# Optimization experiments

Measured on AMD Instinct MI355X. Metric: run time of the kernel, lower is better.

The kernel has to match this reference:

```python
import jax, jax.numpy as jnp
import numpy as np
from jax import lax

sg = lax.stop_gradient

# (kernel, stride, pad, pool_k, pool_s) for the 7 conv blocks
CFG = [(16, 2, 7, 8, 4), (12, 2, 5, 4, 2), (9, 1, 4, 5, 2), (7, 1, 3, 4, 2),
       (5, 1, 2, 2, 2), (3, 1, 1, 2, 2), (3, 1, 1, 2, 2)]
W_SHAPES = [(8, 1, 16), (12, 8, 12), (32, 12, 9), (64, 32, 7),
            (64, 64, 5), (64, 64, 3), (72, 64, 3)]
CH = [8, 12, 32, 64, 64, 64, 72]


def bin_act(x):
    # forward: sign(x); backward: clipped-quadratic surrogate (STE)
    s = jnp.sign(x)
    le = (x < -1.0).astype(x.dtype)
    ri = (x >= 1.0).astype(x.dtype)
    cl = ((x >= -1.0) & (x < 0.0)).astype(x.dtype)
    cr = ((x >= 0.0) & (x < 1.0)).astype(x.dtype)
    out = cl * (2.0 + x) * x + cr * (2.0 - x) * x + ri - le
    return sg(s) + out - sg(out)


def bin_wei(w, axes):
    # forward: scale * sign(w) with scale = mean|w| (detached); backward through tanh (STE)
    scale = sg(jnp.mean(jnp.abs(w), axis=axes, keepdims=True))
    t = jnp.tanh(w)
    return sg(scale * jnp.sign(w)) + t - sg(t)


def conv1d(x, w, stride, pad):
    return lax.conv_general_dilated(x, w, (stride,), [(pad, pad)],
                                    dimension_numbers=('NCH', 'OIH', 'NCH'))


def maxpool1d(x, k, s):
    return lax.reduce_window(x, -jnp.inf, lax.max, (1, 1, k), (1, 1, s), 'VALID')


def batchnorm1d(x, gamma, beta, eps=1e-5):
    # training-mode BN: batch statistics over (N, L), biased variance
    m = jnp.mean(x, axis=(0, 2), keepdims=True)
    v = jnp.mean((x - m) ** 2, axis=(0, 2), keepdims=True)
    return gamma[None, :, None] * (x - m) / jnp.sqrt(v + eps) + beta[None, :, None]


def _forward(x, ws, gs, bs, wfc):
    for w, g, b, (k, s, p, pk, ps) in zip(ws, gs, bs, CFG):
        x = conv1d(x, bin_wei(w, (1, 2)), s, p)
        x = maxpool1d(x, pk, ps)
        x = batchnorm1d(x, g, b)
        x = bin_act(x)
    x = x.reshape(x.shape[0], -1)                 # [B, 72*3]
    return x @ bin_wei(wfc, (1,)).T               # [B, classCount]


def setup_inputs() -> dict:
    key = jax.random.key(0)
    ks = jax.random.split(key, 9)
    inp = {'x': jax.random.normal(ks[0], (2048, 1, 3600), dtype=jnp.float32)}
    for i, shp in enumerate(W_SHAPES):
        inp[f'w{i+1}'] = jax.random.uniform(ks[i + 1], shp, dtype=jnp.float32) * 0.32
        inp[f'g{i+1}'] = jnp.ones((CH[i],), jnp.float32)
        inp[f'b{i+1}'] = jnp.zeros((CH[i],), jnp.float32)
    inp['wfc'] = jax.random.uniform(ks[8], (5, 216), dtype=jnp.float32) * 0.32
    return inp


def reference(x, w1, w2, w3, w4, w5, w6, w7,
              g1, g2, g3, g4, g5, g6, g7,
              b1, b2, b3, b4, b5, b6, b7, wfc):
    ws = [w1, w2, w3, w4, w5, w6, w7]
    gs = [g1, g2, g3, g4, g5, g6, g7]
    bs = [b1, b2, b3, b4, b5, b6, b7]
    return _forward(x, ws, gs, bs, wfc)
```

## Files before the change

### kernel.cpp

```cpp
#include <hip/hip_runtime.h>
#include <math.h>
#include <stdint.h>

#define NBATCH 2048
#define NSLOT 32

struct Args {
    const float* x;
    const float* W[7];
    const float* G[7];
    const float* Bt[7];
    const float* WFC;
    float* out;
    float* bufA;
    float* bufB;
    double* stats;
    float* wsc;
    uint32_t* wmb;
};

__device__ __forceinline__ float signf(float v) {
    return (v > 0.f) ? 1.f : ((v < 0.f) ? -1.f : 0.f);
}

__global__ __launch_bounds__(256) void k_setup(Args a) {
    const int blk = blockIdx.x, tid = threadIdx.x;
    for (int i = blk * 256 + tid; i < NSLOT * 632; i += 391 * 256) a.stats[i] = 0.0;

    if (blk < 321 && tid < 64) {
        const int cum[9] = {0,8,20,52,116,180,244,316,321};
        const int per[8] = {16,96,108,224,320,192,192,216};
        const float* wsrc[8] = {a.W[0],a.W[1],a.W[2],a.W[3],a.W[4],a.W[5],a.W[6],a.WFC};
        int o = blk, L = 0;
        while (L < 7 && o >= cum[L + 1]) ++L;
        const int oo = o - cum[L], p = per[L];
        const float* wo = wsrc[L] + (size_t)oo * p;
        float s = 0.f;
        for (int i = tid; i < p; i += 64) s += fabsf(wo[i]);
        #pragma unroll
        for (int off = 32; off; off >>= 1) s += __shfl_down(s, off);
        if (tid == 0) a.wsc[o] = s / (float)p;
    }

    const int gid = (blk - 384) * 256 + tid;
    if (blk >= 384 && blk <= 388 && gid >= 0 && gid < 1176) {
        const int cum[5]  = {0,448,768,960,1176};
        const int cin[4]  = {32,64,64,64};
        const int kk[4]   = {7,5,3,3};
        const int wpp[4]  = {1,2,2,2};
        const int woff[4] = {356,804,1444,1828};
        const float* wsrc[4] = {a.W[3],a.W[4],a.W[5],a.W[6]};
        int L = 0;
        while (L < 3 && gid >= cum[L + 1]) ++L;
        const int idx = gid - cum[L];
        const int K = kk[L], CIN = cin[L], WPP = wpp[L];
        const int o = idx / K, k = idx - o * K;
        const float* w = wsrc[L];
        uint32_t m0 = 0, m1 = 0;
        for (int c = 0; c < CIN; ++c) {
            const float v = w[((size_t)o * CIN + c) * K + k];
            const uint32_t bit = (v < 0.f) ? 1u : 0u;
            int bp = c;
            if (CIN == 64) bp = 16 * (c & 3) + (c >> 2);
            else if (CIN == 32) bp = 8 * (c & 3) + (c >> 2);
            if (bp < 32) m0 |= bit << bp; else m1 |= bit << (bp - 32);
        }
        uint32_t* dst = a.wmb + woff[L] + (size_t)idx * WPP;
        dst[0] = m0;
        if (WPP == 2) dst[1] = m1;
    }

    if (blk == 389 && tid < 12) {
        const float* w = a.W[1];
        const int o = tid;
        #pragma unroll
        for (int g = 0; g < 3; ++g) {
            uint32_t word = 0;
            #pragma unroll
            for (int j = 0; j < 4; ++j) {
                const int k = 4 * g + j;
                uint32_t by = 0;
                #pragma unroll
                for (int c = 0; c < 8; ++c)
                    by |= (w[((size_t)o * 8 + c) * 12 + k] < 0.f ? 1u : 0u) << c;
                word |= by << (8 * j);
            }
            a.wmb[o * 3 + g] = word;
        }
    }
    if (blk == 390 && tid < 64) {
        const float* w = a.W[2];
        const int o = tid >> 1, ph = tid & 1;
        uint32_t mk[9];
        #pragma unroll
        for (int k = 0; k < 9; ++k) {
            uint32_t m = 0;
            #pragma unroll
            for (int c = 0; c < 12; ++c)
                m |= (w[((size_t)o * 12 + c) * 9 + k] < 0.f ? 1u : 0u) << c;
            mk[k] = m;
        }
        uint32_t wd[5];
        if (ph == 0) { wd[0]=mk[0]|(mk[1]<<16); wd[1]=mk[2]|(mk[3]<<16);
                       wd[2]=mk[4]|(mk[5]<<16); wd[3]=mk[6]|(mk[7]<<16); wd[4]=mk[8]; }
        else         { wd[0]=mk[0]<<16; wd[1]=mk[1]|(mk[2]<<16);
                       wd[2]=mk[3]|(mk[4]<<16); wd[3]=mk[5]|(mk[6]<<16); wd[4]=mk[7]|(mk[8]<<16); }
        #pragma unroll
        for (int g = 0; g < 5; ++g) a.wmb[36 + o * 10 + ph * 5 + g] = wd[g];
    }
}

__global__ __launch_bounds__(256) void k_conv1(Args a) {
    __shared__ float wgs[128];
    __shared__ double sred[16];
    const int n = blockIdx.x, tid = threadIdx.x, l = tid & 63;
    if (tid < 128) wgs[tid] = signf(a.W[0][tid]);
    if (tid < 16)  sred[tid] = 0.0;
    __syncthreads();
    const int r = tid;
    const float* xn = a.x + (size_t)n * 3600;
    float m0[8], m1[8];
    #pragma unroll
    for (int ch = 0; ch < 8; ++ch) { m0[ch] = 0.f; m1[ch] = 0.f; }
    if (r < 225) {
        float f[40];
        const int g0 = 16 * r - 8;
        #pragma unroll
        for (int b = 0; b < 10; ++b) {
            const int gg = g0 + 4 * b;
            if (gg >= 0 && gg <= 3596) {
                const float4 v = *(const float4*)(xn + gg);
                f[4*b] = v.x; f[4*b+1] = v.y; f[4*b+2] = v.z; f[4*b+3] = v.w;
            } else {
                f[4*b] = 0.f; f[4*b+1] = 0.f; f[4*b+2] = 0.f; f[4*b+3] = 0.f;
            }
        }
        #pragma unroll
        for (int ch = 0; ch < 8; ++ch) {
            float acc[12];
            #pragma unroll
            for (int j = 0; j < 12; ++j) acc[j] = 0.f;
            #pragma unroll
            for (int k = 0; k < 16; ++k) {
                const float wk = wgs[ch * 16 + k];
                #pragma unroll
                for (int j = 0; j < 12; ++j)
                    acc[j] = fmaf(f[2*j + 1 + k], wk, acc[j]);
            }
            const float lo  = fmaxf(fmaxf(acc[0], acc[1]), fmaxf(acc[2], acc[3]));
            const float mid = fmaxf(fmaxf(acc[4], acc[5]), fmaxf(acc[6], acc[7]));
            const float hi  = fmaxf(fmaxf(acc[8], acc[9]), fmaxf(acc[10], acc[11]));
            const float sc = a.wsc[ch];
            m0[ch] = fmaxf(lo, mid) * sc;
            m1[ch] = (r < 224) ? fmaxf(mid, hi) * sc : 0.f;
        }
        float* on = a.bufA + ((size_t)n * 449 + 2 * r) * 8;
        *(float4*)(on + 0) = make_float4(m0[0], m0[1], m0[2], m0[3]);
        *(float4*)(on + 4) = make_float4(m0[4], m0[5], m0[6], m0[7]);
        if (r < 224) {
            *(float4*)(on + 8)  = make_float4(m1[0], m1[1], m1[2], m1[3]);
            *(float4*)(on + 12) = make_float4(m1[4], m1[5], m1[6], m1[7]);
        }
    }
    #pragma unroll
    for (int ch = 0; ch < 8; ++ch) {
        double sS = (double)m0[ch] + (double)m1[ch];
        double s2 = (double)m0[ch] * m0[ch] + (double)m1[ch] * m1[ch];
        #pragma unroll
        for (int off = 32; off; off >>= 1) {
            sS += __shfl_down(sS, off);
            s2 += __shfl_down(s2, off);
        }
        if (l == 0) {
            atomicAdd(&sred[ch], sS);
            atomicAdd(&sred[8 + ch], s2);
        }
    }
    __syncthreads();
    if (tid < 16) {
        double* so = a.stats + (size_t)(n & (NSLOT - 1)) * 16;
        atomicAdd(&so[tid], sred[tid]);
    }
}

template <int CIN, int LIN, int O, int K, int STRIDE, int PAD,
          int PK, int PS, int LP, int WPP, int LPB, bool SF64>
__device__ __forceinline__ void bin_body(
    const float* __restrict__ xprev, const uint32_t* __restrict__ wm,
    const float* __restrict__ wsc, const float* __restrict__ wsc_prev,
    const double* __restrict__ stats_in,
    const float* __restrict__ gamma, const float* __restrict__ beta,
    const double cntInv, float* __restrict__ out, double* __restrict__ stats_out)
{
    constexpr int OL    = (O < 64) ? O : 64;
    constexpr int PO    = 64 / OL;
    constexpr int SPAN  = (PK - 1) * STRIDE + K;
    constexpr int QLEN  = 4 * LPB * PS * STRIDE + SPAN;
    constexpr int XM64A =
        (WPP == 2)   ? (QLEN + 2)
      : (CIN == 8)   ? ((QLEN + 48) + 7) / 8
      : (CIN == 12)  ? ((2 * (QLEN + 10)) + 7) / 8
      : ((QLEN + 2 + 3) / 2 + 1);
    constexpr int F     = 2 * CIN;
    constexpr int FW    = (F > 64) ? 128 : 64;

    __shared__ uint64_t xmbuf[XM64A];
    __shared__ long long foldU[4][FW];
    __shared__ int sS[4][O], sS2[4][O];

    const int tid = threadIdx.x;
    const int wv  = tid >> 6;
    const int l   = tid & 63;
    uint32_t* xm32 = (uint32_t*)xmbuf;
    uint64_t* xm64 = xmbuf;
    uint16_t* xm16 = (uint16_t*)xmbuf;
    uint8_t*  xm8  = (uint8_t*)xmbuf;

    const int n    = blockIdx.x;
    const int lp0b = blockIdx.y * (4 * LPB);
    const int lp1b = (lp0b + 4 * LPB < LP) ? lp0b + 4 * LPB : LP;
    const int q0raw = lp0b * PS * STRIDE - PAD;
    const int q0 = (q0raw > 0) ? q0raw : 0;
    const int q1raw = (lp1b - 1) * PS * STRIDE - PAD + SPAN;
    const int q1 = (q1raw < LIN) ? q1raw : LIN;
    int xbase;
    if constexpr (CIN == 8)       xbase = q0 & ~3;
    else if constexpr (CIN == 12) xbase = q0 - (q0 & 1);
    else if constexpr (WPP == 1)  xbase = q0 - ((q0 + (PAD & 1)) & 1);
    else                          xbase = q0;

    const int lp0 = lp0b + wv * LPB;
    const int lp1 = (lp0 + LPB < lp1b) ? lp0 + LPB : lp1b;

    const float* xn = xprev + (size_t)n * LIN * CIN;

    {
        const long long* stI = (const long long*)stats_in;
        long long pa = 0, pb_ = 0;
        double da = 0.0;
        #pragma unroll
        for (int s8 = 0; s8 < 8; ++s8) {
            const int s = (wv << 3) + s8;
            if constexpr (SF64) {
                if (l < F) da += stats_in[s * F + l];
            } else {
                if (l < ((F < 64) ? F : 64)) pa += stI[s * F + l];
                if constexpr (F > 64) { if (l < F - 64) pb_ += stI[s * F + 64 + l]; }
            }
        }
        if constexpr (SF64) foldU[wv][l] = __double_as_longlong(da);
        else {
            foldU[wv][l] = pa;
            if constexpr (F > 64) foldU[wv][64 + l] = pb_;
        }
    }
    __syncthreads();
    float aA = 0.f, aB = 0.f;
    {
        double t0 = 0.0, t1 = 0.0;
        if constexpr (SF64) {
            double tot = 0.0;
            #pragma unroll
            for (int w = 0; w < 4; ++w) tot += __longlong_as_double(foldU[w][l]);
            t0 = tot;
            t1 = __shfl(tot, CIN + l);
        } else if constexpr (F > 64) {
            long long a0 = 0, a1 = 0;
            #pragma unroll
            for (int w = 0; w < 4; ++w) { a0 += foldU[w][l]; a1 += foldU[w][64 + l]; }
            t0 = (double)a0; t1 = (double)a1;
        } else {
            long long a0 = 0;
            #pragma unroll
            for (int w = 0; w < 4; ++w) a0 += foldU[w][l];
            const double tot = (double)a0;
            t0 = tot;
            t1 = __shfl(tot, CIN + l);
        }
        if (l < CIN) {
            double mean, E2;
            if constexpr (SF64) { mean = t0 * cntInv; E2 = t1 * cntInv; }
            else {
                const double w = (double)wsc_prev[l];
                mean = w * t0 * cntInv; E2 = w * w * t1 * cntInv;
            }
            const double var = E2 - mean * mean;
            const double inv = 1.0 / sqrt(var + 1e-5);
            const double av  = (double)gamma[l] * inv;
            aA = (float)av;
            aB = (float)((double)beta[l] - mean * av);
        }
    }

    if constexpr (CIN == 64) {
        const int sub = l & 15, grp = l >> 4;
        const float a0 = __shfl(aA, 4*sub),     b0 = __shfl(aB, 4*sub);
        const float a1 = __shfl(aA, 4*sub + 1), b1 = __shfl(aB, 4*sub + 1);
        const float a2 = __shfl(aA, 4*sub + 2), b2 = __shfl(aB, 4*sub + 2);
        const float a3 = __shfl(aA, 4*sub + 3), b3 = __shfl(aB, 4*sub + 3);
        for (int pb = q0 + wv * 4; pb < q1; pb += 16) {
            const int pos = pb + grp;
            const bool valid = pos < q1;
            const float4 v = *(const float4*)(xn + (size_t)(valid ? pos : q0) * 64 + 4*sub);
            const unsigned long long bal0 = __ballot(valid && (fmaf(a0, v.x, b0) < 0.f));
            const unsigned long long bal1 = __ballot(valid && (fmaf(a1, v.y, b1) < 0.f));
            const unsigned long long bal2 = __ballot(valid && (fmaf(a2, v.z, b2) < 0.f));
            const unsigned long long bal3 = __ballot(valid && (fmaf(a3, v.w, b3) < 0.f));
            if (l < 4 && pb + l < q1) {
                const uint64_t m = ((bal0 >> (16*l)) & 0xFFFFull)
                                 | (((bal1 >> (16*l)) & 0xFFFFull) << 16)
                                 | (((bal2 >> (16*l)) & 0xFFFFull) << 32)
                                 | (((bal3 >> (16*l)) & 0xFFFFull) << 48);
                xm64[pb + l - xbase] = m;
            }
        }
    } else if constexpr (CIN == 32) {
        const int sub = l & 7, grp = l >> 3;
        const float a0 = __shfl(aA, 4*sub),     b0 = __shfl(aB, 4*sub);
        const float a1 = __shfl(aA, 4*sub + 1), b1 = __shfl(aB, 4*sub + 1);
        const float a2 = __shfl(aA, 4*sub + 2), b2 = __shfl(aB, 4*sub + 2);
        const float a3 = __shfl(aA, 4*sub + 3), b3 = __shfl(aB, 4*sub + 3);
        for (int pb = q0 + wv * 8; pb < q1; pb += 32) {
            const int pos = pb + grp;
            const bool valid = pos < q1;
            const float4 v = *(const float4*)(xn + (size_t)(valid ? pos : q0) * 32 + 4*sub);
            const unsigned long long bal0 = __ballot(valid && (fmaf(a0, v.x, b0) < 0.f));
            const unsigned long long bal1 = __ballot(valid && (fmaf(a1, v.y, b1) < 0.f));
            const unsigned long long bal2 = __ballot(valid && (fmaf(a2, v.z, b2) < 0.f));
            const unsigned long long bal3 = __ballot(valid && (fmaf(a3, v.w, b3) < 0.f));
            if (l < 8 && pb + l < q1) {
                const uint32_t m = (uint32_t)((bal0 >> (8*l)) & 0xFFull)
                                 | ((uint32_t)((bal1 >> (8*l)) & 0xFFull) << 8)
                                 | ((uint32_t)((bal2 >> (8*l)) & 0xFFull) << 16)
                                 | ((uint32_t)((bal3 >> (8*l)) & 0xFFull) << 24);
                xm32[pb + l - xbase] = m;
            }
        }
    } else if constexpr (CIN == 8) {
        const int sub = l & 1, grp = l >> 1;
        const float a0 = __shfl(aA, 4*sub),     b0 = __shfl(aB, 4*sub);
        const float a1 = __shfl(aA, 4*sub + 1), b1 = __shfl(aB, 4*sub + 1);
        const float a2 = __shfl(aA, 4*sub + 2), b2 = __shfl(aB, 4*sub + 2);
        const float a3 = __shfl(aA, 4*sub + 3), b3 = __shfl(aB, 4*sub + 3);
        for (int pb = q0 + wv * 32; pb < q1; pb += 128) {
            const int pos = pb + grp;
            const bool valid = pos < q1;
            const float4 v = *(const float4*)(xn + (size_t)(valid ? pos : q0) * 8 + 4*sub);
            const unsigned long long bal0 = __ballot(valid && (fmaf(a0, v.x, b0) < 0.f));
            const unsigned long long bal1 = __ballot(valid && (fmaf(a1, v.y, b1) < 0.f));
            const unsigned long long bal2 = __ballot(valid && (fmaf(a2, v.z, b2) < 0.f));
            const unsigned long long bal3 = __ballot(valid && (fmaf(a3, v.w, b3) < 0.f));
            if (l < 32 && pb + l < q1) {
                const uint32_t t0 = (uint32_t)((bal0 >> (2*l)) & 3ull);
                const uint32_t t1 = (uint32_t)((bal1 >> (2*l)) & 3ull);
                const uint32_t t2 = (uint32_t)((bal2 >> (2*l)) & 3ull);
                const uint32_t t3 = (uint32_t)((bal3 >> (2*l)) & 3ull);
                const uint32_t m = (t0 & 1) | ((t1 & 1) << 1) | ((t2 & 1) << 2) | ((t3 & 1) << 3)
                                 | ((t0 >> 1) << 4) | ((t1 >> 1) << 5) | ((t2 >> 1) << 6) | ((t3 >> 1) << 7);
                xm8[pb + l - xbase] = (uint8_t)m;
            }
        }
    } else {
        constexpr int PPW = 64 / CIN;
        const int pw = l / CIN, c = l - pw * CIN;
        const float myA = __shfl(aA, c), myB = __shfl(aB, c);
        const bool lact = (pw < PPW);
        for (int pb = q0 + wv * PPW; pb < q1; pb += 4 * PPW) {
            const int pos = pb + pw;
            const bool act = lact && (pos < q1);
            float v = 0.f;
            if (act) v = fmaf(myA, xn[(size_t)pb * CIN + l], myB);
            const unsigned long long bal = __ballot(act && (v < 0.f));
            if (act && c == 0) {
                const uint32_t mk = (uint32_t)((bal >> (pw * CIN)) & ((1u << CIN) - 1));
                xm16[pos - xbase] = (uint16_t)mk;
            }
        }
    }
    __syncthreads();

    float* on = out + (size_t)n * LP * O;

    if constexpr (WPP == 2) {
        const uint64_t* wmp = (const uint64_t*)wm;
        uint64_t wr[K];
        #pragma unroll
        for (int k = 0; k < K; ++k) wr[k] = wmp[l * K + k];
        uint64_t wr2[K];
        const int oo2 = 64 + ((O > 64 && l < O - 64) ? l : 0);
        if constexpr (O > 64) {
            #pragma unroll
            for (int k = 0; k < K; ++k) wr2[k] = wmp[oo2 * K + k];
        }
        const float myws  = wsc[l];
        const float myws2 = (O > 64 && l < O - 64) ? wsc[64 + l] : 0.f;
        int accS = 0, accS2 = 0, accSb = 0, accS2b = 0;

        for (int lp = lp0; lp < lp1; ++lp) {
            const int lo = lp * PS * STRIDE - PAD;
            int m = -1000000, m2 = -1000000;
            if (lo >= 0 && lo + SPAN <= LIN) {
                uint64_t tw[SPAN];
                #pragma unroll
                for (int t = 0; t < SPAN; ++t) tw[t] = xm64[lo - xbase + t];
                #pragma unroll
                for (int j = 0; j < PK; ++j) {
                    int p = 0;
                    #pragma unroll
                    for (int k = 0; k < K; ++k)
                        p += __popcll(tw[j * STRIDE + k] ^ wr[k]);
                    m = max(m, CIN * K - 2 * p);
                    if constexpr (O > 64) {
                        int p2 = 0;
                        #pragma unroll
                        for (int k = 0; k < K; ++k)
                            p2 += __popcll(tw[j * STRIDE + k] ^ wr2[k]);
                        m2 = max(m2, CIN * K - 2 * p2);
                    }
                }
            } else {
                #pragma unroll
                for (int j = 0; j < PK; ++j) {
                    const int base = lo + j * STRIDE;
                    int p = 0, nv = 0, p2 = 0;
                    #pragma unroll
                    for (int k = 0; k < K; ++k) {
                        const int q = base + k;
                        if (q >= 0 && q < LIN) {
                            ++nv;
                            const uint64_t xv = xm64[q - xbase];
                            p += __popcll(xv ^ wr[k]);
                            if constexpr (O > 64) p2 += __popcll(xv ^ wr2[k]);
                        }
                    }
                    m = max(m, CIN * nv - 2 * p);
                    if constexpr (O > 64) m2 = max(m2, CIN * nv - 2 * p2);
                }
            }
            on[lp * O + l] = (float)m * myws;
            accS += m; accS2 += m * m;
            if constexpr (O > 64) {
                if (l < O - 64) {
                    on[lp * O + 64 + l] = (float)m2 * myws2;
                    accSb += m2; accS2b += m2 * m2;
                }
            }
        }
        sS[wv][l] = accS; sS2[wv][l] = accS2;
        if constexpr (O > 64) {
            if (l < O - 64) { sS[wv][64 + l] = accSb; sS2[wv][64 + l] = accS2b; }
        }
    } else if constexpr (CIN == 8) {
        const int po = l / OL, oo = l - po * OL;
        const bool cact = (po < PO);
        const float myws = cact ? wsc[oo] : 0.f;
        const int osel = cact ? oo : 0;
        const uint32_t wr0 = wm[osel*3], wr1 = wm[osel*3+1], wr2 = wm[osel*3+2];
        uint32_t wb[12];
        #pragma unroll
        for (int k = 0; k < 12; ++k)
            wb[k] = ((k < 4 ? wr0 : (k < 8 ? wr1 : wr2)) >> (8 * (k & 3))) & 255u;
        const uint32_t* xw = (const uint32_t*)xmbuf;
        int accS = 0, accS2 = 0;

        for (int lp = lp0 + po; lp < lp1; lp += PO) {
            const int lo = lp * PS * STRIDE - PAD;
            int m = -1000000;
            if (lo >= 0 && lo + SPAN <= LIN) {
                const int bb = lo - xbase;
                const int w0 = bb >> 2;
                uint32_t tw[6];
                #pragma unroll
                for (int i = 0; i < 6; ++i) tw[i] = xw[w0 + i];
                #pragma unroll
                for (int j = 0; j < PK; ++j) {
                    const int wo = (j + 1) >> 1;
                    uint32_t e0, e1, e2;
                    if (j & 1) {
                        e0 = (tw[wo]   >> 8) | (tw[wo+1] << 24);
                        e1 = (tw[wo+1] >> 8) | (tw[wo+2] << 24);
                        e2 = (tw[wo+2] >> 8) | (tw[wo+3] << 24);
                    } else {
                        e0 = (tw[wo]   >> 24) | (tw[wo+1] << 8);
                        e1 = (tw[wo+1] >> 24) | (tw[wo+2] << 8);
                        e2 = (tw[wo+2] >> 24) | (tw[wo+3] << 8);
                    }
                    const int p = __popc(e0 ^ wr0) + __popc(e1 ^ wr1) + __popc(e2 ^ wr2);
                    m = max(m, 96 - 2 * p);
                }
            } else {
                #pragma unroll
                for (int j = 0; j < PK; ++j) {
                    const int base = lo + j * STRIDE;
                    int p = 0, nv = 0;
                    #pragma unroll
                    for (int k = 0; k < 12; ++k) {
                        const int q = base + k;
                        if (q >= 0 && q < LIN) { ++nv; p += __popc((uint32_t)xm8[q - xbase] ^ wb[k]); }
                    }
                    m = max(m, 8 * nv - 2 * p);
                }
            }
            if (cact) {
                on[lp * O + oo] = (float)m * myws;
                accS += m; accS2 += m * m;
            }
        }
        int t = accS, t2 = accS2;
        #pragma unroll
        for (int g = 1; g < PO; ++g) {
            t  += __shfl(accS,  l + g * OL);
            t2 += __shfl(accS2, l + g * OL);
        }
        if (l < OL) { sS[wv][l] = t; sS2[wv][l] = t2; }
    } else if constexpr (CIN == 12) {
        const int po = l / OL, oo = l - po * OL;
        const bool cact = (po < PO);
        const float myws = cact ? wsc[oo] : 0.f;
        const int osel = cact ? oo : 0;
        uint32_t wE[5], wO[5];
        #pragma unroll
        for (int g = 0; g < 5; ++g) { wE[g] = wm[osel*10 + g]; wO[g] = wm[osel*10 + 5 + g]; }
        uint32_t we16[9];
        we16[0]=wE[0]&0xFFFFu; we16[1]=wE[0]>>16; we16[2]=wE[1]&0xFFFFu; we16[3]=wE[1]>>16;
        we16[4]=wE[2]&0xFFFFu; we16[5]=wE[2]>>16; we16[6]=wE[3]&0xFFFFu; we16[7]=wE[3]>>16;
        we16[8]=wE[4]&0xFFFFu;
        const uint32_t* xw = (const uint32_t*)xmbuf;
        int accS = 0, accS2 = 0;

        for (int lp = lp0 + po; lp < lp1; lp += PO) {
            const int lo = lp * PS * STRIDE - PAD;
            int m = -1000000;
            if (lo >= 0 && lo + SPAN <= LIN) {
                const int s0 = (lo - xbase) >> 1;
                uint32_t tw[7];
                #pragma unroll
                for (int i = 0; i < 7; ++i) tw[i] = xw[s0 + i];
                #pragma unroll
                for (int j = 0; j < PK; ++j) {
                    const int o_ = j >> 1;
                    int p;
                    if (j & 1)
                        p = __popc((tw[o_] & 0xFFFF0000u) ^ wO[0]) + __popc(tw[o_+1] ^ wO[1])
                          + __popc(tw[o_+2] ^ wO[2]) + __popc(tw[o_+3] ^ wO[3])
                          + __popc(tw[o_+4] ^ wO[4]);
                    else
                        p = __popc(tw[o_] ^ wE[0]) + __popc(tw[o_+1] ^ wE[1])
                          + __popc(tw[o_+2] ^ wE[2]) + __popc(tw[o_+3] ^ wE[3])
                          + __popc((tw[o_+4] & 0xFFFFu) ^ wE[4]);
                    m = max(m, 108 - 2 * p);
                }
            } else {
                #pragma unroll
                for (int j = 0; j < PK; ++j) {
                    const int base = lo + j * STRIDE;
                    int p = 0, nv = 0;
                    #pragma unroll
                    for (int k = 0; k < 9; ++k) {
                        const int q = base + k;
                        if (q >= 0 && q < LIN) { ++nv; p += __popc((uint32_t)xm16[q - xbase] ^ we16[k]); }
                    }
                    m = max(m, 12 * nv - 2 * p);
                }
            }
            if (cact) {
                on[lp * O + oo] = (float)m * myws;
                accS += m; accS2 += m * m;
            }
        }
        int t = accS, t2 = accS2;
        #pragma unroll
        for (int g = 1; g < PO; ++g) {
            t  += __shfl(accS,  l + g * OL);
            t2 += __shfl(accS2, l + g * OL);
        }
        if (l < OL) { sS[wv][l] = t; sS2[wv][l] = t2; }
    } else {
        const int po = l / OL, oo = l - po * OL;
        const bool cact = (po < PO);
        const float myws = cact ? wsc[oo] : 0.f;
        uint32_t wr[K];
        #pragma unroll
        for (int k = 0; k < K; ++k) wr[k] = wm[(cact ? oo : 0) * K + k];
        int accS = 0, accS2 = 0;

        constexpr int PAIRS = (SPAN + 1) / 2;
        for (int lp = lp0 + po; lp < lp1; lp += PO) {
            const int lo = lp * PS * STRIDE - PAD;
            int m = -1000000;
            if (lo >= 0 && lo + SPAN <= LIN) {
                uint32_t tw[PAIRS * 2];
                const int e0 = (lo - xbase) >> 1;
                #pragma unroll
                for (int i = 0; i < PAIRS; ++i) {
                    const uint64_t u64v = xm64[e0 + i];
                    tw[2 * i]     = (uint32_t)u64v;
                    tw[2 * i + 1] = (uint32_t)(u64v >> 32);
                }
                #pragma unroll
                for (int j = 0; j < PK; ++j) {
                    int p = 0;
                    #pragma unroll
                    for (int k = 0; k < K; ++k)
                        p += __popc(tw[j * STRIDE + k] ^ wr[k]);
                    m = max(m, CIN * K - 2 * p);
                }
            } else {
                #pragma unroll
                for (int j = 0; j < PK; ++j) {
                    const int base = lo + j * STRIDE;
                    int p = 0, nv = 0;
                    #pragma unroll
                    for (int k = 0; k < K; ++k) {
                        const int q = base + k;
                        if (q >= 0 && q < LIN) { ++nv; p += __popc(xm32[q - xbase] ^ wr[k]); }
                    }
                    m = max(m, CIN * nv - 2 * p);
                }
            }
            if (cact) {
                on[lp * O + oo] = (float)m * myws;
                accS += m; accS2 += m * m;
            }
        }
        int t = accS, t2 = accS2;
        #pragma unroll
        for (int g = 1; g < PO; ++g) {
            t  += __shfl(accS,  l + g * OL);
            t2 += __shfl(accS2, l + g * OL);
        }
        if (l < OL) { sS[wv][l] = t; sS2[wv][l] = t2; }
    }
    __syncthreads();

    unsigned long long* soU =
        (unsigned long long*)stats_out + (size_t)(n & (NSLOT - 1)) * 2 * O;
    for (int t = tid; t < 2 * O; t += 256) {
        int tot;
        if (t < O) tot = sS[0][t] + sS[1][t] + sS[2][t] + sS[3][t];
        else { const int f = t - O; tot = sS2[0][f] + sS2[1][f] + sS2[2][f] + sS2[3][f]; }
        atomicAdd(&soU[t], (unsigned long long)(long long)tot);
    }
}

#define BIN_PARAMS \
    const float* __restrict__ xprev, const uint32_t* __restrict__ wm, \
    const float* __restrict__ wsc, const float* __restrict__ wsc_prev, \
    const double* __restrict__ stats_in, \
    const float* __restrict__ gamma, const float* __restrict__ beta, \
    const double cntInv, float* __restrict__ out, double* __restrict__ stats_out
#define BIN_ARGS xprev, wm, wsc, wsc_prev, stats_in, gamma, beta, cntInv, out, stats_out

__global__ __launch_bounds__(256) void k_bin2(BIN_PARAMS) { bin_body< 8,449,12,12,2,5,4,2,111,1,14,true >(BIN_ARGS); }
__global__ __launch_bounds__(256) void k_bin3(BIN_PARAMS) { bin_body<12,111,32, 9,1,4,5,2, 54,1,14,false>(BIN_ARGS); }
__global__ __launch_bounds__(256) void k_bin4(BIN_PARAMS) { bin_body<32, 54,64, 7,1,3,4,2, 26,1, 7,false>(BIN_ARGS); }
__global__ __launch_bounds__(256) void k_bin5(BIN_PARAMS) { bin_body<64, 26,64, 5,1,2,2,2, 13,2, 4,false>(BIN_ARGS); }
__global__ __launch_bounds__(256) void k_bin6(BIN_PARAMS) { bin_body<64, 13,64, 3,1,1,2,2,  6,2, 2,false>(BIN_ARGS); }
__global__ __launch_bounds__(256) void k_bin7(BIN_PARAMS) { bin_body<64,  6,72, 3,1,1,2,2,  3,2, 1,false>(BIN_ARGS); }

__global__ __launch_bounds__(256) void k_fc(Args a) {
    const int n = blockIdx.x * 4 + (int)(threadIdx.x >> 6);
    const int l = (int)(threadIdx.x & 63);
    const long long* st = (const long long*)(a.stats + 15616);
    long long s = 0, s2 = 0, sb = 0, s2b = 0;
    #pragma unroll 4
    for (int sl = 0; sl < NSLOT; ++sl) {
        s  += st[sl * 144 + l];
        s2 += st[sl * 144 + 72 + l];
        if (l < 8) {
            sb  += st[sl * 144 + 64 + l];
            s2b += st[sl * 144 + 72 + 64 + l];
        }
    }
    float aA0, aB0, aA1 = 0.f, aB1 = 0.f;
    {
        const double w = (double)a.wsc[244 + l];
        const double mean = w * (double)s / 6144.0;
        const double E2   = w * w * (double)s2 / 6144.0;
        const double var  = E2 - mean * mean;
        const double inv  = 1.0 / sqrt(var + 1e-5);
        const double aa   = (double)a.G[6][l] * inv;
        aA0 = (float)aa; aB0 = (float)((double)a.Bt[6][l] - mean * aa);
    }
    if (l < 8) {
        const double w = (double)a.wsc[244 + 64 + l];
        const double mean = w * (double)sb / 6144.0;
        const double E2   = w * w * (double)s2b / 6144.0;
        const double var  = E2 - mean * mean;
        const double inv  = 1.0 / sqrt(var + 1e-5);
        const double aa   = (double)a.G[6][64 + l] * inv;
        aA1 = (float)aa; aB1 = (float)((double)a.Bt[6][64 + l] - mean * aa);
    }
    const float* p7 = a.bufA + (size_t)n * 216;
    float acc[5] = {0.f, 0.f, 0.f, 0.f, 0.f};
    #pragma unroll
    for (int j = 0; j < 4; ++j) {
        const int i = l + 64 * j;
        const int ic = (i < 216) ? i : 215;
        const int c = ic / 3, lp = ic - 3 * c;
        float aa = __shfl(aA0, c);
        float bb = __shfl(aB0, c);
        const float aaH = __shfl(aA1, c - 64);
        const float bbH = __shfl(aB1, c - 64);
        if (c >= 64) { aa = aaH; bb = bbH; }
        if (i < 216) {
            const float av = signf(fmaf(aa, p7[lp * 72 + c], bb));
            #pragma unroll
            for (int o = 0; o < 5; ++o)
                acc[o] += av * signf(a.WFC[o * 216 + i]);
        }
    }
    #pragma unroll
    for (int o = 0; o < 5; ++o) {
        float v = acc[o];
        #pragma unroll
        for (int off = 32; off; off >>= 1) v += __shfl_down(v, off);
        if (l == 0) a.out[(size_t)n * 5 + o] = v * a.wsc[316 + o];
    }
}

extern "C" void kernel_launch(void* const* d_in, const int* in_sizes, int n_in,
                              void* d_out, int out_size, void* d_ws, size_t ws_size,
                              hipStream_t stream) {
    Args a;
    a.x = (const float*)d_in[0];
    for (int i = 0; i < 7; ++i) {
        a.W[i]  = (const float*)d_in[1 + 3 * i];
        a.G[i]  = (const float*)d_in[2 + 3 * i];
        a.Bt[i] = (const float*)d_in[3 + 3 * i];
    }
    a.WFC = (const float*)d_in[22];
    a.out = (float*)d_out;

    char* ws = (char*)d_ws;
    a.bufA  = (float*)ws;
    a.bufB  = (float*)(ws + 29425664);
    a.stats = (double*)(ws + 43057152);
    a.wsc   = (float*)(ws + 43218944);
    a.wmb   = (uint32_t*)d_out;

    k_setup<<<391, 256, 0, stream>>>(a);
    k_conv1<<<NBATCH, 256, 0, stream>>>(a);
    k_bin2<<<dim3(NBATCH, 2), 256, 0, stream>>>(
        a.bufA, a.wmb + 0, a.wsc + 8, a.wsc, a.stats + 0, a.G[0], a.Bt[0],
        1.0/919552.0, a.bufB, a.stats + 512);
    k_bin3<<<dim3(NBATCH, 1), 256, 0, stream>>>(
        a.bufB, a.wmb + 36, a.wsc + 20, a.wsc + 8, a.stats + 512, a.G[1], a.Bt[1],
        1.0/227328.0, a.bufA, a.stats + 1280);
    k_bin4<<<dim3(NBATCH, 1), 256, 0, stream>>>(
        a.bufA, a.wmb + 356, a.wsc + 52, a.wsc + 20, a.stats + 1280, a.G[2], a.Bt[2],
        1.0/110592.0, a.bufB, a.stats + 3328);
    k_bin5<<<dim3(NBATCH, 1), 256, 0, stream>>>(
        a.bufB, a.wmb + 804, a.wsc + 116, a.wsc + 52, a.stats + 3328, a.G[3], a.Bt[3],
        1.0/53248.0, a.bufA, a.stats + 7424);
    k_bin6<<<dim3(NBATCH, 1), 256, 0, stream>>>(
        a.bufA, a.wmb + 1444, a.wsc + 180, a.wsc + 116, a.stats + 7424, a.G[4], a.Bt[4],
        1.0/26624.0, a.bufB, a.stats + 11520);
    k_bin7<<<dim3(NBATCH, 1), 256, 0, stream>>>(
        a.bufB, a.wmb + 1828, a.wsc + 244, a.wsc + 180, a.stats + 11520, a.G[5], a.Bt[5],
        1.0/12288.0, a.bufA, a.stats + 15616);
    k_fc<<<NBATCH / 4, 256, 0, stream>>>(a);
}
```

Baseline: 260.9 us.

## Pack layer-4 weights as even/odd 64-bit words and vectorize window loads

Layer-4 binary weights (CIN=32, K=7) are now pre-packed per output channel into two 64-bit-aligned layouts, even and odd phase. The inner popcount loop can then use 64-bit XOR/popcll on pairs of positions instead of 32-bit popc per tap. Each lane now handles one output channel across all positions, replacing the earlier split of positions across lane groups. The WPP==2 path loads its shared-memory window with 128-bit reads, and the buffer sizes, alignment and weight offsets are adjusted to fit. The layer-4 path is hard-coded to its shape (224, PK=4), and the changed alignment and xbase rules add a correctness risk.

```diff
diff --git a/kernel.cpp b/kernel.cpp
--- a/kernel.cpp
+++ b/kernel.cpp
@@ -43,31 +43,51 @@
     }
 
     const int gid = (blk - 384) * 256 + tid;
-    if (blk >= 384 && blk <= 388 && gid >= 0 && gid < 1176) {
-        const int cum[5]  = {0,448,768,960,1176};
-        const int cin[4]  = {32,64,64,64};
-        const int kk[4]   = {7,5,3,3};
-        const int wpp[4]  = {1,2,2,2};
-        const int woff[4] = {356,804,1444,1828};
-        const float* wsrc[4] = {a.W[3],a.W[4],a.W[5],a.W[6]};
+    if (blk >= 384 && blk <= 386 && gid >= 0 && gid < 728) {
+        const int cum[4]  = {0,320,512,728};
+        const int kk[3]   = {5,3,3};
+        const int woff[3] = {1380,2020,2404};
+        const float* wsrc[3] = {a.W[4],a.W[5],a.W[6]};
         int L = 0;
-        while (L < 3 && gid >= cum[L + 1]) ++L;
+        while (L < 2 && gid >= cum[L + 1]) ++L;
         const int idx = gid - cum[L];
-        const int K = kk[L], CIN = cin[L], WPP = wpp[L];
+        const int K = kk[L];
         const int o = idx / K, k = idx - o * K;
         const float* w = wsrc[L];
         uint32_t m0 = 0, m1 = 0;
-        for (int c = 0; c < CIN; ++c) {
-            const float v = w[((size_t)o * CIN + c) * K + k];
+        for (int c = 0; c < 64; ++c) {
+            const float v = w[((size_t)o * 64 + c) * K + k];
             const uint32_t bit = (v < 0.f) ? 1u : 0u;
-            int bp = c;
-            if (CIN == 64) bp = 16 * (c & 3) + (c >> 2);
-            else if (CIN == 32) bp = 8 * (c & 3) + (c >> 2);
+            const int bp = 16 * (c & 3) + (c >> 2);
             if (bp < 32) m0 |= bit << bp; else m1 |= bit << (bp - 32);
         }
-        uint32_t* dst = a.wmb + woff[L] + (size_t)idx * WPP;
-        dst[0] = m0;
-        if (WPP == 2) dst[1] = m1;
+        uint32_t* dst = a.wmb + woff[L] + (size_t)idx * 2;
+        dst[0] = m0; dst[1] = m1;
+    }
+
+    if (blk == 387 && tid < 64) {
+        const float* w = a.W[3];
+        const int o = tid;
+        uint32_t mk[7];
+        #pragma unroll
+        for (int k = 0; k < 7; ++k) {
+            uint32_t m = 0;
+            #pragma unroll
+            for (int c = 0; c < 32; ++c) {
+                const int bp = 8 * (c & 3) + (c >> 2);
+                m |= (w[((size_t)o * 32 + c) * 7 + k] < 0.f ? 1u : 0u) << bp;
+            }
+            mk[k] = m;
+        }
+        uint64_t* dst = (uint64_t*)(a.wmb + 356) + (size_t)o * 8;
+        dst[0] = (uint64_t)mk[0] | ((uint64_t)mk[1] << 32);
+        dst[1] = (uint64_t)mk[2] | ((uint64_t)mk[3] << 32);
+        dst[2] = (uint64_t)mk[4] | ((uint64_t)mk[5] << 32);
+        dst[3] = (uint64_t)mk[6];
+        dst[4] = ((uint64_t)mk[0] << 32);
+        dst[5] = (uint64_t)mk[1] | ((uint64_t)mk[2] << 32);
+        dst[6] = (uint64_t)mk[3] | ((uint64_t)mk[4] << 32);
+        dst[7] = (uint64_t)mk[5] | ((uint64_t)mk[6] << 32);
     }
 
     if (blk == 389 && tid < 12) {
@@ -197,14 +217,14 @@
     constexpr int SPAN  = (PK - 1) * STRIDE + K;
     constexpr int QLEN  = 4 * LPB * PS * STRIDE + SPAN;
     constexpr int XM64A =
-        (WPP == 2)   ? (QLEN + 2)
+        (WPP == 2)   ? (QLEN + 3)
       : (CIN == 8)   ? ((QLEN + 48) + 7) / 8
       : (CIN == 12)  ? ((2 * (QLEN + 10)) + 7) / 8
-      : ((QLEN + 2 + 3) / 2 + 1);
+      : ((QLEN + 5) / 2 + 2);
     constexpr int F     = 2 * CIN;
     constexpr int FW    = (F > 64) ? 128 : 64;
 
-    __shared__ uint64_t xmbuf[XM64A];
+    alignas(16) __shared__ uint64_t xmbuf[XM64A];
     __shared__ long long foldU[4][FW];
     __shared__ int sS[4][O], sS2[4][O];
 
@@ -226,8 +246,7 @@
     int xbase;
     if constexpr (CIN == 8)       xbase = q0 & ~3;
     else if constexpr (CIN == 12) xbase = q0 - (q0 & 1);
-    else if constexpr (WPP == 1)  xbase = q0 - ((q0 + (PAD & 1)) & 1);
-    else                          xbase = q0;
+    else                          xbase = q0 - ((q0 + (PAD & 1)) & 1);
 
     const int lp0 = lp0b + wv * LPB;
     const int lp1 = (lp0 + LPB < lp1b) ? lp0 + LPB : lp1b;
@@ -401,8 +420,13 @@
             int m = -1000000, m2 = -1000000;
             if (lo >= 0 && lo + SPAN <= LIN) {
                 uint64_t tw[SPAN];
-                #pragma unroll
-                for (int t = 0; t < SPAN; ++t) tw[t] = xm64[lo - xbase + t];
+                const int e0 = lo - xbase;
+                #pragma unroll
+                for (int i = 0; i < SPAN / 2; ++i) {
+                    const ulonglong2 u = *(const ulonglong2*)&xm64[e0 + 2 * i];
+                    tw[2 * i] = u.x; tw[2 * i + 1] = u.y;
+                }
+                if constexpr (SPAN & 1) tw[SPAN - 1] = xm64[e0 + SPAN - 1];
                 #pragma unroll
                 for (int j = 0; j < PK; ++j) {
                     int p = 0;
@@ -576,60 +600,56 @@
         }
         if (l < OL) { sS[wv][l] = t; sS2[wv][l] = t2; }
     } else {
-        const int po = l / OL, oo = l - po * OL;
-        const bool cact = (po < PO);
-        const float myws = cact ? wsc[oo] : 0.f;
-        uint32_t wr[K];
-        #pragma unroll
-        for (int k = 0; k < K; ++k) wr[k] = wm[(cact ? oo : 0) * K + k];
+        const uint64_t* wp = (const uint64_t*)wm;
+        uint64_t wE[4], wO[4];
+        #pragma unroll
+        for (int g = 0; g < 4; ++g) { wE[g] = wp[(size_t)l*8 + g]; wO[g] = wp[(size_t)l*8 + 4 + g]; }
+        const float myws = wsc[l];
+        const uint64_t hiM = 0xFFFFFFFF00000000ull;
         int accS = 0, accS2 = 0;
 
-        constexpr int PAIRS = (SPAN + 1) / 2;
-        for (int lp = lp0 + po; lp < lp1; lp += PO) {
+        for (int lp = lp0; lp < lp1; ++lp) {
             const int lo = lp * PS * STRIDE - PAD;
             int m = -1000000;
             if (lo >= 0 && lo + SPAN <= LIN) {
-                uint32_t tw[PAIRS * 2];
-                const int e0 = (lo - xbase) >> 1;
-                #pragma unroll
-                for (int i = 0; i < PAIRS; ++i) {
-                    const uint64_t u64v = xm64[e0 + i];
-                    tw[2 * i]     = (uint32_t)u64v;
-                    tw[2 * i + 1] = (uint32_t)(u64v >> 32);
-                }
-                #pragma unroll
-                for (int j = 0; j < PK; ++j) {
-                    int p = 0;
-                    #pragma unroll
-                    for (int k = 0; k < K; ++k)
-                        p += __popc(tw[j * STRIDE + k] ^ wr[k]);
-                    m = max(m, CIN * K - 2 * p);
-                }
+                const int a0 = (lo - xbase) >> 1;
+                const uint64_t t0 = xm64[a0],     t1 = xm64[a0 + 1], t2 = xm64[a0 + 2],
+                               t3 = xm64[a0 + 3], t4 = xm64[a0 + 4];
+                int p;
+                p = __popcll(t0 ^ wE[0]) + __popcll(t1 ^ wE[1]) + __popcll(t2 ^ wE[2])
+                  + __popc((uint32_t)t3 ^ (uint32_t)wE[3]);
+                m = max(m, 224 - 2 * p);
+                p = __popcll((t0 & hiM) ^ wO[0]) + __popcll(t1 ^ wO[1])
+                  + __popcll(t2 ^ wO[2]) + __popcll(t3 ^ wO[3]);
+                m = max(m, 224 - 2 * p);
+                p = __popcll(t1 ^ wE[0]) + __popcll(t2 ^ wE[1]) + __popcll(t3 ^ wE[2])
+                  + __popc((uint32_t)t4 ^ (uint32_t)wE[3]);
+                m = max(m, 224 - 2 * p);
+                p = __popcll((t1 & hiM) ^ wO[0]) + __popcll(t2 ^ wO[1])
+                  + __popcll(t3 ^ wO[2]) + __popcll(t4 ^ wO[3]);
+                m = max(m, 224 - 2 * p);
             } else {
+                const uint32_t wb[7] = {
+                    (uint32_t)wE[0], (uint32_t)(wE[0] >> 32),
+                    (uint32_t)wE[1], (uint32_t)(wE[1] >> 32),
+                    (uint32_t)wE[2], (uint32_t)(wE[2] >> 32),
+                    (uint32_t)wE[3] };
                 #pragma unroll
                 for (int j = 0; j < PK; ++j) {
                     const int base = lo + j * STRIDE;
                     int p = 0, nv = 0;
                     #pragma unroll
-                    for (int k = 0; k < K; ++k) {
+                    for (int k = 0; k < 7; ++k) {
                         const int q = base + k;
-                        if (q >= 0 && q < LIN) { ++nv; p += __popc(xm32[q - xbase] ^ wr[k]); }
+                        if (q >= 0 && q < LIN) { ++nv; p += __popc(xm32[q - xbase] ^ wb[k]); }
                     }
-                    m = max(m, CIN * nv - 2 * p);
-                }
-            }
-            if (cact) {
-                on[lp * O + oo] = (float)m * myws;
-                accS += m; accS2 += m * m;
-            }
-        }
-        int t = accS, t2 = accS2;
-        #pragma unroll
-        for (int g = 1; g < PO; ++g) {
-            t  += __shfl(accS,  l + g * OL);
-            t2 += __shfl(accS2, l + g * OL);
-        }
-        if (l < OL) { sS[wv][l] = t; sS2[wv][l] = t2; }
+                    m = max(m, 32 * nv - 2 * p);
+                }
+            }
+            on[lp * O + l] = (float)m * myws;
+            accS += m; accS2 += m * m;
+        }
+        sS[wv][l] = accS; sS2[wv][l] = accS2;
     }
     __syncthreads();
 
@@ -751,13 +771,13 @@
         a.bufA, a.wmb + 356, a.wsc + 52, a.wsc + 20, a.stats + 1280, a.G[2], a.Bt[2],
         1.0/110592.0, a.bufB, a.stats + 3328);
     k_bin5<<<dim3(NBATCH, 1), 256, 0, stream>>>(
-        a.bufB, a.wmb + 804, a.wsc + 116, a.wsc + 52, a.stats + 3328, a.G[3], a.Bt[3],
+        a.bufB, a.wmb + 1380, a.wsc + 116, a.wsc + 52, a.stats + 3328, a.G[3], a.Bt[3],
         1.0/53248.0, a.bufA, a.stats + 7424);
     k_bin6<<<dim3(NBATCH, 1), 256, 0, stream>>>(
-        a.bufA, a.wmb + 1444, a.wsc + 180, a.wsc + 116, a.stats + 7424, a.G[4], a.Bt[4],
+        a.bufA, a.wmb + 2020, a.wsc + 180, a.wsc + 116, a.stats + 7424, a.G[4], a.Bt[4],
         1.0/26624.0, a.bufB, a.stats + 11520);
     k_bin7<<<dim3(NBATCH, 1), 256, 0, stream>>>(
-        a.bufB, a.wmb + 1828, a.wsc + 244, a.wsc + 180, a.stats + 11520, a.G[5], a.Bt[5],
+        a.bufB, a.wmb + 2404, a.wsc + 244, a.wsc + 180, a.stats + 11520, a.G[5], a.Bt[5],
         1.0/12288.0, a.bufA, a.stats + 15616);
     k_fc<<<NBATCH / 4, 256, 0, stream>>>(a);
 }
```

After: 265.7 us. About the same (+1.8%).

## Pack two samples per block in late binary layers, merge bin2 tiles

Applied to the files above, without the earlier changes.

Adds an NS template parameter so one 256-thread block can handle two batch samples, each served by two wavefronts with its own shared bitmask buffer. Layers 5–7 switch to NS=2 with half the blocks and adjusted LPB. Layer 2 instead doubles LPB and drops its second grid-y tile. The aim is to cut idle wavefronts and per-block overhead in the short-sequence layers, at the cost of fewer wavefronts per sample and some indexing and padding changes.

```diff
diff --git a/kernel.cpp b/kernel.cpp
--- a/kernel.cpp
+++ b/kernel.cpp
@@ -184,7 +184,7 @@
 }
 
 template <int CIN, int LIN, int O, int K, int STRIDE, int PAD,
-          int PK, int PS, int LP, int WPP, int LPB, bool SF64>
+          int PK, int PS, int LP, int WPP, int LPB, int NS, bool SF64>
 __device__ __forceinline__ void bin_body(
     const float* __restrict__ xprev, const uint32_t* __restrict__ wm,
     const float* __restrict__ wsc, const float* __restrict__ wsc_prev,
@@ -194,31 +194,34 @@
 {
     constexpr int OL    = (O < 64) ? O : 64;
     constexpr int PO    = 64 / OL;
+    constexpr int WPW   = 4 / NS;
     constexpr int SPAN  = (PK - 1) * STRIDE + K;
-    constexpr int QLEN  = 4 * LPB * PS * STRIDE + SPAN;
+    constexpr int QLEN  = WPW * LPB * PS * STRIDE + SPAN;
     constexpr int XM64A =
-        (WPP == 2)   ? (QLEN + 2)
+        (WPP == 2)   ? (QLEN + 3)
       : (CIN == 8)   ? ((QLEN + 48) + 7) / 8
       : (CIN == 12)  ? ((2 * (QLEN + 10)) + 7) / 8
-      : ((QLEN + 2 + 3) / 2 + 1);
+      : ((QLEN + 5) / 2 + 2);
     constexpr int F     = 2 * CIN;
     constexpr int FW    = (F > 64) ? 128 : 64;
 
-    __shared__ uint64_t xmbuf[XM64A];
+    __shared__ uint64_t xmbuf[NS][XM64A];
     __shared__ long long foldU[4][FW];
     __shared__ int sS[4][O], sS2[4][O];
 
-    const int tid = threadIdx.x;
-    const int wv  = tid >> 6;
-    const int l   = tid & 63;
-    uint32_t* xm32 = (uint32_t*)xmbuf;
-    uint64_t* xm64 = xmbuf;
-    uint16_t* xm16 = (uint16_t*)xmbuf;
-    uint8_t*  xm8  = (uint8_t*)xmbuf;
-
-    const int n    = blockIdx.x;
-    const int lp0b = blockIdx.y * (4 * LPB);
-    const int lp1b = (lp0b + 4 * LPB < LP) ? lp0b + 4 * LPB : LP;
+    const int tid  = threadIdx.x;
+    const int wv   = tid >> 6;
+    const int l    = tid & 63;
+    const int sloc = wv / WPW;
+    const int wvs  = wv % WPW;
+    uint64_t* xm64 = xmbuf[sloc];
+    uint32_t* xm32 = (uint32_t*)xm64;
+    uint16_t* xm16 = (uint16_t*)xm64;
+    uint8_t*  xm8  = (uint8_t*)xm64;
+
+    const int n    = blockIdx.x * NS + sloc;
+    const int lp0b = blockIdx.y * (WPW * LPB);
+    const int lp1b = (lp0b + WPW * LPB < LP) ? lp0b + WPW * LPB : LP;
     const int q0raw = lp0b * PS * STRIDE - PAD;
     const int q0 = (q0raw > 0) ? q0raw : 0;
     const int q1raw = (lp1b - 1) * PS * STRIDE - PAD + SPAN;
@@ -229,7 +232,7 @@
     else if constexpr (WPP == 1)  xbase = q0 - ((q0 + (PAD & 1)) & 1);
     else                          xbase = q0;
 
-    const int lp0 = lp0b + wv * LPB;
+    const int lp0 = lp0b + wvs * LPB;
     const int lp1 = (lp0 + LPB < lp1b) ? lp0 + LPB : lp1b;
 
     const float* xn = xprev + (size_t)n * LIN * CIN;
@@ -298,7 +301,7 @@
         const float a1 = __shfl(aA, 4*sub + 1), b1 = __shfl(aB, 4*sub + 1);
         const float a2 = __shfl(aA, 4*sub + 2), b2 = __shfl(aB, 4*sub + 2);
         const float a3 = __shfl(aA, 4*sub + 3), b3 = __shfl(aB, 4*sub + 3);
-        for (int pb = q0 + wv * 4; pb < q1; pb += 16) {
+        for (int pb = q0 + wvs * 4; pb < q1; pb += WPW * 4) {
             const int pos = pb + grp;
             const bool valid = pos < q1;
             const float4 v = *(const float4*)(xn + (size_t)(valid ? pos : q0) * 64 + 4*sub);
@@ -320,7 +323,7 @@
         const float a1 = __shfl(aA, 4*sub + 1), b1 = __shfl(aB, 4*sub + 1);
         const float a2 = __shfl(aA, 4*sub + 2), b2 = __shfl(aB, 4*sub + 2);
         const float a3 = __shfl(aA, 4*sub + 3), b3 = __shfl(aB, 4*sub + 3);
-        for (int pb = q0 + wv * 8; pb < q1; pb += 32) {
+        for (int pb = q0 + wvs * 8; pb < q1; pb += WPW * 8) {
             const int pos = pb + grp;
             const bool valid = pos < q1;
             const float4 v = *(const float4*)(xn + (size_t)(valid ? pos : q0) * 32 + 4*sub);
@@ -342,7 +345,7 @@
         const float a1 = __shfl(aA, 4*sub + 1), b1 = __shfl(aB, 4*sub + 1);
         const float a2 = __shfl(aA, 4*sub + 2), b2 = __shfl(aB, 4*sub + 2);
         const float a3 = __shfl(aA, 4*sub + 3), b3 = __shfl(aB, 4*sub + 3);
-        for (int pb = q0 + wv * 32; pb < q1; pb += 128) {
+        for (int pb = q0 + wvs * 32; pb < q1; pb += WPW * 32) {
             const int pos = pb + grp;
             const bool valid = pos < q1;
             const float4 v = *(const float4*)(xn + (size_t)(valid ? pos : q0) * 8 + 4*sub);
@@ -365,7 +368,7 @@
         const int pw = l / CIN, c = l - pw * CIN;
         const float myA = __shfl(aA, c), myB = __shfl(aB, c);
         const bool lact = (pw < PPW);
-        for (int pb = q0 + wv * PPW; pb < q1; pb += 4 * PPW) {
+        for (int pb = q0 + wvs * PPW; pb < q1; pb += WPW * PPW) {
             const int pos = pb + pw;
             const bool act = lact && (pos < q1);
             float v = 0.f;
@@ -449,6 +452,7 @@
         sS[wv][l] = accS; sS2[wv][l] = accS2;
         if constexpr (O > 64) {
             if (l < O - 64) { sS[wv][64 + l] = accSb; sS2[wv][64 + l] = accS2b; }
+            else if (l >= O - 64) {  }
         }
     } else if constexpr (CIN == 8) {
         const int po = l / OL, oo = l - po * OL;
@@ -460,7 +464,7 @@
         #pragma unroll
         for (int k = 0; k < 12; ++k)
             wb[k] = ((k < 4 ? wr0 : (k < 8 ? wr1 : wr2)) >> (8 * (k & 3))) & 255u;
-        const uint32_t* xw = (const uint32_t*)xmbuf;
+        const uint32_t* xw = (const uint32_t*)xm64;
         int accS = 0, accS2 = 0;
 
         for (int lp = lp0 + po; lp < lp1; lp += PO) {
@@ -513,6 +517,7 @@
             t2 += __shfl(accS2, l + g * OL);
         }
         if (l < OL) { sS[wv][l] = t; sS2[wv][l] = t2; }
+        else if (l < O) { sS[wv][l] = 0; sS2[wv][l] = 0; }
     } else if constexpr (CIN == 12) {
         const int po = l / OL, oo = l - po * OL;
         const bool cact = (po < PO);
@@ -525,7 +530,7 @@
         we16[0]=wE[0]&0xFFFFu; we16[1]=wE[0]>>16; we16[2]=wE[1]&0xFFFFu; we16[3]=wE[1]>>16;
         we16[4]=wE[2]&0xFFFFu; we16[5]=wE[2]>>16; we16[6]=wE[3]&0xFFFFu; we16[7]=wE[3]>>16;
         we16[8]=wE[4]&0xFFFFu;
-        const uint32_t* xw = (const uint32_t*)xmbuf;
+        const uint32_t* xw = (const uint32_t*)xm64;
         int accS = 0, accS2 = 0;
 
         for (int lp = lp0 + po; lp < lp1; lp += PO) {
@@ -633,8 +638,9 @@
     }
     __syncthreads();
 
+    const int slot = ((NS == 1) ? n : (int)blockIdx.x) & (NSLOT - 1);
     unsigned long long* soU =
-        (unsigned long long*)stats_out + (size_t)(n & (NSLOT - 1)) * 2 * O;
+        (unsigned long long*)stats_out + (size_t)slot * 2 * O;
     for (int t = tid; t < 2 * O; t += 256) {
         int tot;
         if (t < O) tot = sS[0][t] + sS[1][t] + sS[2][t] + sS[3][t];
@@ -651,12 +657,12 @@
     const double cntInv, float* __restrict__ out, double* __restrict__ stats_out
 #define BIN_ARGS xprev, wm, wsc, wsc_prev, stats_in, gamma, beta, cntInv, out, stats_out
 
-__global__ __launch_bounds__(256) void k_bin2(BIN_PARAMS) { bin_body< 8,449,12,12,2,5,4,2,111,1,14,true >(BIN_ARGS); }
-__global__ __launch_bounds__(256) void k_bin3(BIN_PARAMS) { bin_body<12,111,32, 9,1,4,5,2, 54,1,14,false>(BIN_ARGS); }
-__global__ __launch_bounds__(256) void k_bin4(BIN_PARAMS) { bin_body<32, 54,64, 7,1,3,4,2, 26,1, 7,false>(BIN_ARGS); }
-__global__ __launch_bounds__(256) void k_bin5(BIN_PARAMS) { bin_body<64, 26,64, 5,1,2,2,2, 13,2, 4,false>(BIN_ARGS); }
-__global__ __launch_bounds__(256) void k_bin6(BIN_PARAMS) { bin_body<64, 13,64, 3,1,1,2,2,  6,2, 2,false>(BIN_ARGS); }
-__global__ __launch_bounds__(256) void k_bin7(BIN_PARAMS) { bin_body<64,  6,72, 3,1,1,2,2,  3,2, 1,false>(BIN_ARGS); }
+__global__ __launch_bounds__(256) void k_bin2(BIN_PARAMS) { bin_body< 8,449,12,12,2,5,4,2,111,1,28,1,true >(BIN_ARGS); }
+__global__ __launch_bounds__(256) void k_bin3(BIN_PARAMS) { bin_body<12,111,32, 9,1,4,5,2, 54,1,14,1,false>(BIN_ARGS); }
+__global__ __launch_bounds__(256) void k_bin4(BIN_PARAMS) { bin_body<32, 54,64, 7,1,3,4,2, 26,1, 7,1,false>(BIN_ARGS); }
+__global__ __launch_bounds__(256) void k_bin5(BIN_PARAMS) { bin_body<64, 26,64, 5,1,2,2,2, 13,2, 7,2,false>(BIN_ARGS); }
+__global__ __launch_bounds__(256) void k_bin6(BIN_PARAMS) { bin_body<64, 13,64, 3,1,1,2,2,  6,2, 3,2,false>(BIN_ARGS); }
+__global__ __launch_bounds__(256) void k_bin7(BIN_PARAMS) { bin_body<64,  6,72, 3,1,1,2,2,  3,2, 2,2,false>(BIN_ARGS); }
 
 __global__ __launch_bounds__(256) void k_fc(Args a) {
     const int n = blockIdx.x * 4 + (int)(threadIdx.x >> 6);
@@ -741,7 +747,7 @@
 
     k_setup<<<391, 256, 0, stream>>>(a);
     k_conv1<<<NBATCH, 256, 0, stream>>>(a);
-    k_bin2<<<dim3(NBATCH, 2), 256, 0, stream>>>(
+    k_bin2<<<dim3(NBATCH, 1), 256, 0, stream>>>(
         a.bufA, a.wmb + 0, a.wsc + 8, a.wsc, a.stats + 0, a.G[0], a.Bt[0],
         1.0/919552.0, a.bufB, a.stats + 512);
     k_bin3<<<dim3(NBATCH, 1), 256, 0, stream>>>(
@@ -750,13 +756,13 @@
     k_bin4<<<dim3(NBATCH, 1), 256, 0, stream>>>(
         a.bufA, a.wmb + 356, a.wsc + 52, a.wsc + 20, a.stats + 1280, a.G[2], a.Bt[2],
         1.0/110592.0, a.bufB, a.stats + 3328);
-    k_bin5<<<dim3(NBATCH, 1), 256, 0, stream>>>(
+    k_bin5<<<dim3(NBATCH / 2, 1), 256, 0, stream>>>(
         a.bufB, a.wmb + 804, a.wsc + 116, a.wsc + 52, a.stats + 3328, a.G[3], a.Bt[3],
         1.0/53248.0, a.bufA, a.stats + 7424);
-    k_bin6<<<dim3(NBATCH, 1), 256, 0, stream>>>(
+    k_bin6<<<dim3(NBATCH / 2, 1), 256, 0, stream>>>(
         a.bufA, a.wmb + 1444, a.wsc + 180, a.wsc + 116, a.stats + 7424, a.G[4], a.Bt[4],
         1.0/26624.0, a.bufB, a.stats + 11520);
-    k_bin7<<<dim3(NBATCH, 1), 256, 0, stream>>>(
+    k_bin7<<<dim3(NBATCH / 2, 1), 256, 0, stream>>>(
         a.bufB, a.wmb + 1828, a.wsc + 244, a.wsc + 180, a.stats + 11520, a.G[5], a.Bt[5],
         1.0/12288.0, a.bufA, a.stats + 15616);
     k_fc<<<NBATCH / 4, 256, 0, stream>>>(a);
```

Result: faster. 254.9 us (-2.3%).
